# Performance work log

Hardware: AMD Instinct MI355X
Metric: run time of the kernel (lower is better)

Reference implementation:

```python
import jax, jax.numpy as jnp
import numpy as np

EPS = 1e-4
HEADS = 16
DH = 64


def setup_inputs() -> dict:
    key = jax.random.key(0)
    ks = jax.random.split(key, 5)
    b, t, d = 2, 2048, 1024
    return {
        "X": jax.random.normal(ks[0], (b, t, d), dtype=jnp.float32),
        "W_in": jax.random.normal(ks[1], (HEADS * 4 * DH, d), dtype=jnp.float32) * (1.0 / np.sqrt(d)),
        "b_in": jax.random.normal(ks[2], (HEADS * 4 * DH,), dtype=jnp.float32) * 0.01,
        "W_out": jax.random.normal(ks[3], (d, HEADS * DH), dtype=jnp.float32) * (1.0 / np.sqrt(HEADS * DH)),
        "b_out": jax.random.normal(ks[4], (d,), dtype=jnp.float32) * 0.01,
    }


def reference(X, W_in, b_in, W_out, b_out):
    b, t, d = X.shape
    # project_in: [b,t,h*4*dh] -> [b,t,h,4*dh] -> [b,h,t,4*dh]
    P = jnp.einsum('btd,ed->bte', X, W_in) + b_in
    P = P.reshape(b, t, HEADS, 4 * DH).transpose(0, 2, 1, 3)
    Q, K, V, G = jnp.split(P, 4, axis=-1)  # each [b,h,t,dh]
    # Euclidean cdist: sqrt(||q||^2 + ||k||^2 - 2 q.k), clamped at 0
    q2 = jnp.sum(Q * Q, axis=-1)[..., :, None]   # [b,h,t,1]
    k2 = jnp.sum(K * K, axis=-1)[..., None, :]   # [b,h,1,t]
    qk = jnp.einsum('bhqd,bhkd->bhqk', Q, K)
    dist = jnp.sqrt(jnp.maximum(q2 + k2 - 2.0 * qk, 0.0))
    # Shepard weights: (eps + dist)^-2, normalized over keys
    W = (EPS + dist) ** (-2)
    W = W / (EPS + jnp.sum(W, axis=-1, keepdims=True))
    A = jnp.einsum('bhqk,bhkd->bhqd', W, V)
    # gate, merge heads: [b,h,t,dh] -> [b,t,h*dh]
    H = (G * A).transpose(0, 2, 1, 3).reshape(b, t, HEADS * DH)
    Y = jnp.einsum('bte,de->btd', H, W_out) + b_out
    return Y
```

## Files before the change

kernel.cpp:

```cpp
#include <hip/hip_runtime.h>
#include <math.h>

#define EPS 1e-4f


typedef __attribute__((ext_vector_type(8))) short bf16x8;
typedef __attribute__((ext_vector_type(8))) unsigned short u16x8;
typedef __attribute__((ext_vector_type(4))) float f32x4;

#define MFMA(a, b, c) __builtin_amdgcn_mfma_f32_16x16x32_bf16(a, b, c, 0, 0, 0)

__device__ __forceinline__ unsigned short f2b(float f) {
    unsigned int u = __float_as_uint(f);
    u += 0x7fffu + ((u >> 16) & 1u);
    return (unsigned short)(u >> 16);
}
__device__ __forceinline__ float b2f(unsigned short u) {
    return __uint_as_float(((unsigned int)u) << 16);
}
__device__ __forceinline__ unsigned int cvtpk(float a, float b) {
    unsigned int r;
    asm("v_cvt_pk_bf16_f32 %0, %1, %2" : "=v"(r) : "v"(a), "v"(b));
    return r;
}

typedef __attribute__((address_space(1))) const unsigned int as1_u32;
typedef __attribute__((address_space(3))) unsigned int as3_u32;
__device__ __forceinline__ void gl_lds16(const unsigned short* g, unsigned short* l) {
    __builtin_amdgcn_global_load_lds((as1_u32*)g, (as3_u32*)l, 16, 0, 0);
}

__global__ __launch_bounds__(256)
void sga_f2b(const float* __restrict__ src, unsigned short* __restrict__ dst, int n8) {
    int i = blockIdx.x * 256 + threadIdx.x;
    const int stride = gridDim.x * 256;
    for (; i < n8; i += stride) {
        const float4* s = (const float4*)src + i * 2;
        float4 a = s[0], b = s[1];
        uint4 o;
        o.x = (unsigned)f2b(a.x) | ((unsigned)f2b(a.y) << 16);
        o.y = (unsigned)f2b(a.z) | ((unsigned)f2b(a.w) << 16);
        o.z = (unsigned)f2b(b.x) | ((unsigned)f2b(b.y) << 16);
        o.w = (unsigned)f2b(b.z) | ((unsigned)f2b(b.w) << 16);
        *((uint4*)dst + i) = o;
    }
}

__global__ __launch_bounds__(256)
void sga_gemm1(const unsigned short* __restrict__ Xb, const unsigned short* __restrict__ Wb,
               const float* __restrict__ bin,
               unsigned short* __restrict__ Qb, unsigned short* __restrict__ Kb,
               unsigned short* __restrict__ Vt, unsigned short* __restrict__ Gb,
               float* __restrict__ q2s, float* __restrict__ k2s)
{
    __shared__ unsigned short As[128 * 64];
    __shared__ unsigned short Bs[128 * 64];
    const int tid = threadIdx.x;
    const int lane = tid & 63, w = tid >> 6;
    const int lr = lane & 15, lg = lane >> 4;
    const int wm = w & 1, wn = w >> 1;
    const int m0 = blockIdx.y * 128, n0 = blockIdx.x * 128;

    const int sr = tid >> 3, sc8 = tid & 7;
    const int gch = sc8 ^ (sr & 7);
    const unsigned short* aBase = Xb + (m0 + sr) * 1024 + gch * 8;
    const unsigned short* bBase = Wb + (n0 + sr) * 1024 + gch * 8;
    unsigned short* aDst = &As[w * 512];
    unsigned short* bDst = &Bs[w * 512];

    f32x4 acc[4][4] = {};

    for (int kt = 0; kt < 16; ++kt) {
        __syncthreads();
        #pragma unroll
        for (int c = 0; c < 4; ++c)
            gl_lds16(aBase + c * 32768 + kt * 64, aDst + c * 2048);
        #pragma unroll
        for (int c = 0; c < 4; ++c)
            gl_lds16(bBase + c * 32768 + kt * 64, bDst + c * 2048);
        __syncthreads();

        #pragma unroll
        for (int ks = 0; ks < 2; ++ks) {
            bf16x8 af[4], bfr[4];
            #pragma unroll
            for (int i = 0; i < 4; ++i) {
                const int row = wm * 64 + i * 16 + lr;
                af[i] = *(const bf16x8*)&As[row * 64 + (((ks * 4 + lg) ^ (row & 7)) * 8)];
            }
            #pragma unroll
            for (int i = 0; i < 4; ++i) {
                const int row = wn * 64 + i * 16 + lr;
                bfr[i] = *(const bf16x8*)&Bs[row * 64 + (((ks * 4 + lg) ^ (row & 7)) * 8)];
            }
            #pragma unroll
            for (int mi = 0; mi < 4; ++mi)
                #pragma unroll
                for (int ni = 0; ni < 4; ++ni)
                    acc[mi][ni] = MFMA(af[mi], bfr[ni], acc[mi][ni]);
        }
    }

    const int bb = m0 >> 11;
    const bool qkBlock = ((n0 & 128) == 0);
    #pragma unroll
    for (int mf = 0; mf < 4; ++mf) {
        const int tbase = m0 + wm * 64 + mf * 16 + lg * 4;
        const int tloc = tbase & 2047;
        float s2[4] = {0.f, 0.f, 0.f, 0.f};
        #pragma unroll
        for (int nf = 0; nf < 4; ++nf) {
            const int n = n0 + wn * 64 + nf * 16 + lr;
            const int h = n >> 8, cc = n & 255;
            const int part = cc >> 6, j = cc & 63;
            const int bh = bb * 16 + h;
            const float bz = bin[n];
            f32x4 v = acc[mf][nf];
            unsigned short e0 = f2b(v[0] + bz), e1 = f2b(v[1] + bz),
                           e2 = f2b(v[2] + bz), e3 = f2b(v[3] + bz);
            if (qkBlock) {
                float f0 = b2f(e0), f1 = b2f(e1), f2 = b2f(e2), f3 = b2f(e3);
                s2[0] += f0 * f0; s2[1] += f1 * f1;
                s2[2] += f2 * f2; s2[3] += f3 * f3;
            }
            if (part == 2) {
                ushort4 pk = make_ushort4(e0, e1, e2, e3);
                *(ushort4*)&Vt[(bh * 64 + j) * 2048 + tloc] = pk;
            } else {
                unsigned short* dst = (part == 0) ? Qb : ((part == 1) ? Kb : Gb);
                unsigned short vv[4] = {e0, e1, e2, e3};
                #pragma unroll
                for (int r = 0; r < 4; ++r)
                    dst[(bh * 2048 + tloc + r) * 64 + j] = vv[r];
            }
        }
        if (qkBlock) {
            const int bh = bb * 16 + (n0 >> 8);
            float* __restrict__ dstn = wn ? k2s : q2s;
            #pragma unroll
            for (int r = 0; r < 4; ++r) {
                float v = s2[r];
                v += __shfl_xor(v, 1, 64); v += __shfl_xor(v, 2, 64);
                v += __shfl_xor(v, 4, 64); v += __shfl_xor(v, 8, 64);
                if (lr == 0) dstn[bh * 2048 + ((tloc + r) & 2047)] = v;
            }
        }
    }
}

__global__ __launch_bounds__(256, 3)
void sga_attn(const unsigned short* __restrict__ Qb, const unsigned short* __restrict__ Kb,
              const unsigned short* __restrict__ Vt,
              const float* __restrict__ q2s, const float* __restrict__ k2s,
              unsigned short* __restrict__ Op0, unsigned short* __restrict__ Op1,
              unsigned short* __restrict__ Op2,
              float* __restrict__ Sw0, float* __restrict__ Sw1, float* __restrict__ Sw2)
{
    __shared__ unsigned short Klds[2 * 4096];
    __shared__ unsigned short Vlds[2 * 4096];
    __shared__ unsigned short Wlds[4 * 2048];

    const int tid = threadIdx.x;
    const int lane = tid & 63, w = tid >> 6;
    const int lr = lane & 15, lg = lane >> 4;

    const int qt = blockIdx.x, bh = blockIdx.y, half = blockIdx.z;
    const int q0 = qt * 128 + w * 32;
    const int kbeg = half * 11;
    const int kend = (half == 2) ? 32 : (kbeg + 11);

    unsigned short* wl = &Wlds[w * 2048];
    unsigned short* __restrict__ Op = (half == 0) ? Op0 : ((half == 1) ? Op1 : Op2);
    float* __restrict__ Sw = (half == 0) ? Sw0 : ((half == 1) ? Sw1 : Sw2);

    const int srow = w * 16 + (lane >> 2);
    const int sc = (lane & 3) * 2;
    const unsigned short* Kg = Kb + (bh * 2048 + srow) * 64 + sc * 8;
    const unsigned short* Vg = Vt + (bh * 64 + srow) * 2048 + sc * 8;
    const int swz0 = srow * 64 + ((sc ^ (srow & 7)) * 8);
    const int swz1 = srow * 64 + (((sc + 1) ^ (srow & 7)) * 8);

    bf16x8 qf[2][2];
    #pragma unroll
    for (int g = 0; g < 2; ++g) {
        const unsigned short* qp = Qb + (bh * 2048 + q0 + g * 16 + lr) * 64 + lg * 8;
        qf[g][0] = *(const bf16x8*)qp;
        qf[g][1] = *(const bf16x8*)(qp + 32);
    }
    float q2v[2];
    q2v[0] = q2s[bh * 2048 + q0 + lr];
    q2v[1] = q2s[bh * 2048 + q0 + 16 + lr];

    f32x4 oacc[2][4] = {};
    float sumw[2] = {0.f, 0.f};

    uint4 ks0, ks1, vs0, vs1;
    {
        const unsigned short* kp = Kg + kbeg * 4096;
        ks0 = *(const uint4*)kp; ks1 = *(const uint4*)(kp + 8);
        const unsigned short* vp = Vg + kbeg * 64;
        vs0 = *(const uint4*)vp; vs1 = *(const uint4*)(vp + 8);
    }
    *(uint4*)&Klds[swz0] = ks0; *(uint4*)&Klds[swz1] = ks1;
    *(uint4*)&Vlds[swz0] = vs0; *(uint4*)&Vlds[swz1] = vs1;
    __syncthreads();

    int buf = 0;
    for (int kt = kbeg; kt < kend; ++kt) {
        const int k0 = kt * 64;
        const bool more = (kt + 1 < kend);

        if (more) {
            const unsigned short* kp = Kg + (kt + 1) * 4096;
            ks0 = *(const uint4*)kp; ks1 = *(const uint4*)(kp + 8);
            const unsigned short* vp = Vg + (kt + 1) * 64;
            vs0 = *(const uint4*)vp; vs1 = *(const uint4*)(vp + 8);
        }

        f32x4 k2v[4];
        #pragma unroll
        for (int nf = 0; nf < 4; ++nf)
            k2v[nf] = *(const f32x4*)&k2s[bh * 2048 + k0 + nf * 16 + lg * 4];

        f32x4 sa[2][4] = {};
        const unsigned short* kb = &Klds[buf * 4096];
        __builtin_amdgcn_s_setprio(1);
        #pragma unroll
        for (int nf = 0; nf < 4; ++nf) {
            const int row = nf * 16 + lr;
            bf16x8 kf0 = *(const bf16x8*)&kb[row * 64 + ((lg ^ (row & 7)) * 8)];
            bf16x8 kf1 = *(const bf16x8*)&kb[row * 64 + (((4 + lg) ^ (row & 7)) * 8)];
            #pragma unroll
            for (int g = 0; g < 2; ++g) {
                sa[g][nf] = MFMA(kf0, qf[g][0], sa[g][nf]);
                sa[g][nf] = MFMA(kf1, qf[g][1], sa[g][nf]);
            }
        }
        __builtin_amdgcn_s_setprio(0);

        #pragma unroll
        for (int g = 0; g < 2; ++g) {
            const int row = g * 16 + lr;
            #pragma unroll
            for (int nf = 0; nf < 4; ++nf) {
                float wv[4];
                #pragma unroll
                for (int r = 0; r < 4; ++r) {
                    float d2 = fmaf(-2.0f, sa[g][nf][r], q2v[g] + k2v[nf][r]);
                    d2 = fmaxf(d2, 1e-8f);
                    wv[r] = __builtin_amdgcn_rcpf(d2);
                    sumw[g] += wv[r];
                }
                uint2 pk;
                pk.x = cvtpk(wv[0], wv[1]);
                pk.y = cvtpk(wv[2], wv[3]);
                const int c = 2 * nf + (lg >> 1);
                *(uint2*)&wl[row * 64 + ((c ^ (row & 7)) * 8) + (lg & 1) * 4] = pk;
            }
        }

        bf16x8 pa[2][2];
        #pragma unroll
        for (int g = 0; g < 2; ++g) {
            const int row = g * 16 + lr;
            pa[g][0] = *(const bf16x8*)&wl[row * 64 + ((lg ^ (row & 7)) * 8)];
            pa[g][1] = *(const bf16x8*)&wl[row * 64 + (((4 + lg) ^ (row & 7)) * 8)];
        }
        const unsigned short* vb = &Vlds[buf * 4096];
        __builtin_amdgcn_s_setprio(1);
        #pragma unroll
        for (int vf = 0; vf < 4; ++vf) {
            const int row = vf * 16 + lr;
            bf16x8 v0 = *(const bf16x8*)&vb[row * 64 + ((lg ^ (row & 7)) * 8)];
            bf16x8 v1 = *(const bf16x8*)&vb[row * 64 + (((4 + lg) ^ (row & 7)) * 8)];
            #pragma unroll
            for (int g = 0; g < 2; ++g) {
                oacc[g][vf] = MFMA(pa[g][0], v0, oacc[g][vf]);
                oacc[g][vf] = MFMA(pa[g][1], v1, oacc[g][vf]);
            }
        }
        __builtin_amdgcn_s_setprio(0);

        if (more) {
            const int bo = (buf ^ 1) * 4096;
            *(uint4*)&Klds[bo + swz0] = ks0; *(uint4*)&Klds[bo + swz1] = ks1;
            *(uint4*)&Vlds[bo + swz0] = vs0; *(uint4*)&Vlds[bo + swz1] = vs1;
            __syncthreads();
            buf ^= 1;
        }
    }

    #pragma unroll
    for (int g = 0; g < 2; ++g) {
        sumw[g] += __shfl_xor(sumw[g], 16, 64);
        sumw[g] += __shfl_xor(sumw[g], 32, 64);
    }

    #pragma unroll
    for (int g = 0; g < 2; ++g) {
        #pragma unroll
        for (int vf = 0; vf < 4; ++vf) {
            #pragma unroll
            for (int r = 0; r < 4; ++r) {
                const int t = q0 + g * 16 + lg * 4 + r;
                const int dh = vf * 16 + lr;
                Op[(bh * 2048 + t) * 64 + dh] = f2b(oacc[g][vf][r]);
            }
        }
    }
    if (lg == 0) {
        Sw[bh * 2048 + q0 + lr]      = sumw[0];
        Sw[bh * 2048 + q0 + 16 + lr] = sumw[1];
    }
}

__global__ __launch_bounds__(256)
void sga_combine(const unsigned short* __restrict__ Op0, const unsigned short* __restrict__ Op1,
                 const unsigned short* __restrict__ Op2,
                 const float* __restrict__ Sw0, const float* __restrict__ Sw1,
                 const float* __restrict__ Sw2,
                 const unsigned short* __restrict__ Gb, unsigned short* __restrict__ Hb)
{
    const int idx = blockIdx.x * 256 + threadIdx.x;
    const int t16 = idx >> 3;
    const int dq = (idx & 7) << 3;
    u16x8 a = *(const u16x8*)&Op0[t16 * 64 + dq];
    u16x8 b = *(const u16x8*)&Op1[t16 * 64 + dq];
    u16x8 c = *(const u16x8*)&Op2[t16 * 64 + dq];
    u16x8 g = *(const u16x8*)&Gb[t16 * 64 + dq];
    const float s = Sw0[t16] + Sw1[t16] + Sw2[t16];
    const float inv = __builtin_amdgcn_rcpf(EPS + s);
    const int bh = t16 >> 11, tloc = t16 & 2047;
    const int bb = bh >> 4, h = bh & 15;
    u16x8 o;
    #pragma unroll
    for (int j = 0; j < 8; ++j)
        o[j] = f2b((b2f(a[j]) + b2f(b[j]) + b2f(c[j])) * inv * b2f(g[j]));
    *(u16x8*)&Hb[(bb * 2048 + tloc) * 1024 + h * 64 + dq] = o;
}

__global__ __launch_bounds__(256)
void sga_gemm2(const unsigned short* __restrict__ Hb, const unsigned short* __restrict__ Wb,
               const float* __restrict__ bout, float* __restrict__ Y)
{
    __shared__ unsigned short As[128 * 64];
    __shared__ unsigned short Bs[128 * 64];
    const int tid = threadIdx.x;
    const int lane = tid & 63, w = tid >> 6;
    const int lr = lane & 15, lg = lane >> 4;
    const int wm = w & 1, wn = w >> 1;
    const int m0 = blockIdx.y * 128, n0 = blockIdx.x * 128;

    const int sr = tid >> 3, sc8 = tid & 7;
    const int gch = sc8 ^ (sr & 7);
    const unsigned short* aBase = Hb + (m0 + sr) * 1024 + gch * 8;
    const unsigned short* bBase = Wb + (n0 + sr) * 1024 + gch * 8;
    unsigned short* aDst = &As[w * 512];
    unsigned short* bDst = &Bs[w * 512];

    f32x4 acc[4][4] = {};

    for (int kt = 0; kt < 16; ++kt) {
        __syncthreads();
        #pragma unroll
        for (int c = 0; c < 4; ++c)
            gl_lds16(aBase + c * 32768 + kt * 64, aDst + c * 2048);
        #pragma unroll
        for (int c = 0; c < 4; ++c)
            gl_lds16(bBase + c * 32768 + kt * 64, bDst + c * 2048);
        __syncthreads();

        #pragma unroll
        for (int ks = 0; ks < 2; ++ks) {
            bf16x8 af[4], bfr[4];
            #pragma unroll
            for (int i = 0; i < 4; ++i) {
                const int row = wm * 64 + i * 16 + lr;
                af[i] = *(const bf16x8*)&As[row * 64 + (((ks * 4 + lg) ^ (row & 7)) * 8)];
            }
            #pragma unroll
            for (int i = 0; i < 4; ++i) {
                const int row = wn * 64 + i * 16 + lr;
                bfr[i] = *(const bf16x8*)&Bs[row * 64 + (((ks * 4 + lg) ^ (row & 7)) * 8)];
            }
            #pragma unroll
            for (int mi = 0; mi < 4; ++mi)
                #pragma unroll
                for (int ni = 0; ni < 4; ++ni)
                    acc[mi][ni] = MFMA(af[mi], bfr[ni], acc[mi][ni]);
        }
    }

    #pragma unroll
    for (int mf = 0; mf < 4; ++mf) {
        const int m = m0 + wm * 64 + mf * 16 + lg * 4;
        #pragma unroll
        for (int nf = 0; nf < 4; ++nf) {
            const int n = n0 + wn * 64 + nf * 16 + lr;
            const float bz = bout[n];
            f32x4 v = acc[mf][nf];
            #pragma unroll
            for (int r = 0; r < 4; ++r)
                Y[(m + r) * 1024 + n] = v[r] + bz;
        }
    }
}

extern "C" void kernel_launch(void* const* d_in, const int* in_sizes, int n_in,
                              void* d_out, int out_size, void* d_ws, size_t ws_size,
                              hipStream_t stream) {
    const float* X    = (const float*)d_in[0];
    const float* Win  = (const float*)d_in[1];
    const float* bin  = (const float*)d_in[2];
    const float* Wout = (const float*)d_in[3];
    const float* bout = (const float*)d_in[4];
    float* Y = (float*)d_out;

    const int PER = 32 * 2048 * 64;
    unsigned short* Qb   = (unsigned short*)d_ws;
    unsigned short* Kb   = Qb + PER;
    unsigned short* Vt   = Kb + PER;
    unsigned short* Gb   = Vt + PER;
    unsigned short* Hb   = Gb + PER;
    unsigned short* Xb   = Hb + PER;
    unsigned short* Winb = Xb + PER;
    unsigned short* Woutb= Winb + PER;
    float* q2s = (float*)(Woutb + 1024 * 1024);
    float* k2s = q2s + 32 * 2048;
    float* Sw0 = k2s + 32 * 2048;
    float* Sw1 = Sw0 + 32 * 2048;
    float* Sw2 = Sw1 + 32 * 2048;
    unsigned short* Op2 = (unsigned short*)(Sw2 + 32 * 2048);
    unsigned short* Op0 = Xb;
    unsigned short* Op1 = Winb;

    sga_f2b<<<1024, 256, 0, stream>>>(X, Xb, 524288);
    sga_f2b<<<1024, 256, 0, stream>>>(Win, Winb, 524288);
    sga_f2b<<<256, 256, 0, stream>>>(Wout, Woutb, 131072);
    sga_gemm1<<<dim3(32, 32), 256, 0, stream>>>(Xb, Winb, bin, Qb, Kb, Vt, Gb, q2s, k2s);
    sga_attn <<<dim3(16, 32, 3), 256, 0, stream>>>(Qb, Kb, Vt, q2s, k2s,
                                                   Op0, Op1, Op2, Sw0, Sw1, Sw2);
    sga_combine<<<2048, 256, 0, stream>>>(Op0, Op1, Op2, Sw0, Sw1, Sw2, Gb, Hb);
    sga_gemm2<<<dim3(8, 32), 256, 0, stream>>>(Hb, Woutb, bout, Y);
}
```

Measured before the change: 153.1 us.

## Split attention keys four ways with single-buffered direct-to-LDS loads

The attention kernel now splits the key range into four equal chunks instead of three uneven ones, so the grid holds more blocks. K and V tiles go straight from global memory into a single LDS buffer through a direct load helper, replacing the register-staged double buffer. Launch bounds rise to four blocks per CU to match the smaller LDS footprint. In exchange, loads are no longer overlapped with compute within a block, two barriers are added per tile, and the combine kernel reads an extra partial output.

```diff
diff --git a/kernel.cpp b/kernel.cpp
--- a/kernel.cpp
+++ b/kernel.cpp
@@ -148,16 +148,17 @@
     }
 }
 
-__global__ __launch_bounds__(256, 3)
+__global__ __launch_bounds__(256, 4)
 void sga_attn(const unsigned short* __restrict__ Qb, const unsigned short* __restrict__ Kb,
               const unsigned short* __restrict__ Vt,
               const float* __restrict__ q2s, const float* __restrict__ k2s,
               unsigned short* __restrict__ Op0, unsigned short* __restrict__ Op1,
-              unsigned short* __restrict__ Op2,
-              float* __restrict__ Sw0, float* __restrict__ Sw1, float* __restrict__ Sw2)
+              unsigned short* __restrict__ Op2, unsigned short* __restrict__ Op3,
+              float* __restrict__ Sw0, float* __restrict__ Sw1,
+              float* __restrict__ Sw2, float* __restrict__ Sw3)
 {
-    __shared__ unsigned short Klds[2 * 4096];
-    __shared__ unsigned short Vlds[2 * 4096];
+    __shared__ unsigned short Klds[4096];
+    __shared__ unsigned short Vlds[4096];
     __shared__ unsigned short Wlds[4 * 2048];
 
     const int tid = threadIdx.x;
@@ -166,19 +167,20 @@
 
     const int qt = blockIdx.x, bh = blockIdx.y, half = blockIdx.z;
     const int q0 = qt * 128 + w * 32;
-    const int kbeg = half * 11;
-    const int kend = (half == 2) ? 32 : (kbeg + 11);
+    const int kbeg = half * 8, kend = kbeg + 8;
 
     unsigned short* wl = &Wlds[w * 2048];
-    unsigned short* __restrict__ Op = (half == 0) ? Op0 : ((half == 1) ? Op1 : Op2);
-    float* __restrict__ Sw = (half == 0) ? Sw0 : ((half == 1) ? Sw1 : Sw2);
-
-    const int srow = w * 16 + (lane >> 2);
-    const int sc = (lane & 3) * 2;
-    const unsigned short* Kg = Kb + (bh * 2048 + srow) * 64 + sc * 8;
-    const unsigned short* Vg = Vt + (bh * 64 + srow) * 2048 + sc * 8;
-    const int swz0 = srow * 64 + ((sc ^ (srow & 7)) * 8);
-    const int swz1 = srow * 64 + (((sc + 1) ^ (srow & 7)) * 8);
+    unsigned short* __restrict__ Op =
+        (half & 2) ? ((half & 1) ? Op3 : Op2) : ((half & 1) ? Op1 : Op0);
+    float* __restrict__ Sw =
+        (half & 2) ? ((half & 1) ? Sw3 : Sw2) : ((half & 1) ? Sw1 : Sw0);
+
+    const int sr8 = tid >> 3, sch = tid & 7;
+    const int gch = sch ^ (sr8 & 7);
+    const unsigned short* Kg = Kb + bh * 2048 * 64;
+    const unsigned short* Vg = Vt + bh * 64 * 2048;
+    unsigned short* kDst = &Klds[w * 512];
+    unsigned short* vDst = &Vlds[w * 512];
 
     bf16x8 qf[2][2];
     #pragma unroll
@@ -194,28 +196,17 @@
     f32x4 oacc[2][4] = {};
     float sumw[2] = {0.f, 0.f};
 
-    uint4 ks0, ks1, vs0, vs1;
-    {
-        const unsigned short* kp = Kg + kbeg * 4096;
-        ks0 = *(const uint4*)kp; ks1 = *(const uint4*)(kp + 8);
-        const unsigned short* vp = Vg + kbeg * 64;
-        vs0 = *(const uint4*)vp; vs1 = *(const uint4*)(vp + 8);
-    }
-    *(uint4*)&Klds[swz0] = ks0; *(uint4*)&Klds[swz1] = ks1;
-    *(uint4*)&Vlds[swz0] = vs0; *(uint4*)&Vlds[swz1] = vs1;
-    __syncthreads();
-
-    int buf = 0;
     for (int kt = kbeg; kt < kend; ++kt) {
         const int k0 = kt * 64;
-        const bool more = (kt + 1 < kend);
-
-        if (more) {
-            const unsigned short* kp = Kg + (kt + 1) * 4096;
-            ks0 = *(const uint4*)kp; ks1 = *(const uint4*)(kp + 8);
-            const unsigned short* vp = Vg + (kt + 1) * 64;
-            vs0 = *(const uint4*)vp; vs1 = *(const uint4*)(vp + 8);
-        }
+
+        __syncthreads();
+        #pragma unroll
+        for (int c = 0; c < 2; ++c) {
+            const int row = c * 32 + sr8;
+            gl_lds16(Kg + (k0 + row) * 64 + gch * 8, kDst + c * 2048);
+            gl_lds16(Vg + row * 2048 + k0 + gch * 8, vDst + c * 2048);
+        }
+        __syncthreads();
 
         f32x4 k2v[4];
         #pragma unroll
@@ -223,13 +214,12 @@
             k2v[nf] = *(const f32x4*)&k2s[bh * 2048 + k0 + nf * 16 + lg * 4];
 
         f32x4 sa[2][4] = {};
-        const unsigned short* kb = &Klds[buf * 4096];
         __builtin_amdgcn_s_setprio(1);
         #pragma unroll
         for (int nf = 0; nf < 4; ++nf) {
             const int row = nf * 16 + lr;
-            bf16x8 kf0 = *(const bf16x8*)&kb[row * 64 + ((lg ^ (row & 7)) * 8)];
-            bf16x8 kf1 = *(const bf16x8*)&kb[row * 64 + (((4 + lg) ^ (row & 7)) * 8)];
+            bf16x8 kf0 = *(const bf16x8*)&Klds[row * 64 + ((lg ^ (row & 7)) * 8)];
+            bf16x8 kf1 = *(const bf16x8*)&Klds[row * 64 + (((4 + lg) ^ (row & 7)) * 8)];
             #pragma unroll
             for (int g = 0; g < 2; ++g) {
                 sa[g][nf] = MFMA(kf0, qf[g][0], sa[g][nf]);
@@ -266,13 +256,12 @@
             pa[g][0] = *(const bf16x8*)&wl[row * 64 + ((lg ^ (row & 7)) * 8)];
             pa[g][1] = *(const bf16x8*)&wl[row * 64 + (((4 + lg) ^ (row & 7)) * 8)];
         }
-        const unsigned short* vb = &Vlds[buf * 4096];
         __builtin_amdgcn_s_setprio(1);
         #pragma unroll
         for (int vf = 0; vf < 4; ++vf) {
             const int row = vf * 16 + lr;
-            bf16x8 v0 = *(const bf16x8*)&vb[row * 64 + ((lg ^ (row & 7)) * 8)];
-            bf16x8 v1 = *(const bf16x8*)&vb[row * 64 + (((4 + lg) ^ (row & 7)) * 8)];
+            bf16x8 v0 = *(const bf16x8*)&Vlds[row * 64 + ((lg ^ (row & 7)) * 8)];
+            bf16x8 v1 = *(const bf16x8*)&Vlds[row * 64 + (((4 + lg) ^ (row & 7)) * 8)];
             #pragma unroll
             for (int g = 0; g < 2; ++g) {
                 oacc[g][vf] = MFMA(pa[g][0], v0, oacc[g][vf]);
@@ -280,14 +269,6 @@
             }
         }
         __builtin_amdgcn_s_setprio(0);
-
-        if (more) {
-            const int bo = (buf ^ 1) * 4096;
-            *(uint4*)&Klds[bo + swz0] = ks0; *(uint4*)&Klds[bo + swz1] = ks1;
-            *(uint4*)&Vlds[bo + swz0] = vs0; *(uint4*)&Vlds[bo + swz1] = vs1;
-            __syncthreads();
-            buf ^= 1;
-        }
     }
 
     #pragma unroll
@@ -316,9 +297,9 @@
 
 __global__ __launch_bounds__(256)
 void sga_combine(const unsigned short* __restrict__ Op0, const unsigned short* __restrict__ Op1,
-                 const unsigned short* __restrict__ Op2,
+                 const unsigned short* __restrict__ Op2, const unsigned short* __restrict__ Op3,
                  const float* __restrict__ Sw0, const float* __restrict__ Sw1,
-                 const float* __restrict__ Sw2,
+                 const float* __restrict__ Sw2, const float* __restrict__ Sw3,
                  const unsigned short* __restrict__ Gb, unsigned short* __restrict__ Hb)
 {
     const int idx = blockIdx.x * 256 + threadIdx.x;
@@ -327,15 +308,16 @@
     u16x8 a = *(const u16x8*)&Op0[t16 * 64 + dq];
     u16x8 b = *(const u16x8*)&Op1[t16 * 64 + dq];
     u16x8 c = *(const u16x8*)&Op2[t16 * 64 + dq];
+    u16x8 d = *(const u16x8*)&Op3[t16 * 64 + dq];
     u16x8 g = *(const u16x8*)&Gb[t16 * 64 + dq];
-    const float s = Sw0[t16] + Sw1[t16] + Sw2[t16];
+    const float s = Sw0[t16] + Sw1[t16] + Sw2[t16] + Sw3[t16];
     const float inv = __builtin_amdgcn_rcpf(EPS + s);
     const int bh = t16 >> 11, tloc = t16 & 2047;
     const int bb = bh >> 4, h = bh & 15;
     u16x8 o;
     #pragma unroll
     for (int j = 0; j < 8; ++j)
-        o[j] = f2b((b2f(a[j]) + b2f(b[j]) + b2f(c[j])) * inv * b2f(g[j]));
+        o[j] = f2b((b2f(a[j]) + b2f(b[j]) + b2f(c[j]) + b2f(d[j])) * inv * b2f(g[j]));
     *(u16x8*)&Hb[(bb * 2048 + tloc) * 1024 + h * 64 + dq] = o;
 }
 
@@ -430,7 +412,9 @@
     float* Sw0 = k2s + 32 * 2048;
     float* Sw1 = Sw0 + 32 * 2048;
     float* Sw2 = Sw1 + 32 * 2048;
-    unsigned short* Op2 = (unsigned short*)(Sw2 + 32 * 2048);
+    float* Sw3 = Sw2 + 32 * 2048;
+    unsigned short* Op2 = (unsigned short*)(Sw3 + 32 * 2048);
+    unsigned short* Op3 = Op2 + PER;
     unsigned short* Op0 = Xb;
     unsigned short* Op1 = Winb;
 
@@ -438,8 +422,8 @@
     sga_f2b<<<1024, 256, 0, stream>>>(Win, Winb, 524288);
     sga_f2b<<<256, 256, 0, stream>>>(Wout, Woutb, 131072);
     sga_gemm1<<<dim3(32, 32), 256, 0, stream>>>(Xb, Winb, bin, Qb, Kb, Vt, Gb, q2s, k2s);
-    sga_attn <<<dim3(16, 32, 3), 256, 0, stream>>>(Qb, Kb, Vt, q2s, k2s,
-                                                   Op0, Op1, Op2, Sw0, Sw1, Sw2);
-    sga_combine<<<2048, 256, 0, stream>>>(Op0, Op1, Op2, Sw0, Sw1, Sw2, Gb, Hb);
+    sga_attn <<<dim3(16, 32, 4), 256, 0, stream>>>(Qb, Kb, Vt, q2s, k2s,
+                                                   Op0, Op1, Op2, Op3, Sw0, Sw1, Sw2, Sw3);
+    sga_combine<<<2048, 256, 0, stream>>>(Op0, Op1, Op2, Op3, Sw0, Sw1, Sw2, Sw3, Gb, Hb);
     sga_gemm2<<<dim3(8, 32), 256, 0, stream>>>(Hb, Woutb, bout, Y);
 }
```

Measured after the change: 166.0 us. +8.4%, slower.
